# Performance work log

Measured on AMD Instinct MI355X. Metric: run time of the kernel, lower is better.

The kernel has to match this reference:

```python
import jax, jax.numpy as jnp
import numpy as np

D_K = 64
N_HEADS = 16
D_MODEL = 1024


def setup_inputs() -> dict:
    key = jax.random.key(0)
    ks = jax.random.split(key, 12)
    N, T = 2, 2048
    H = D_K * N_HEADS
    s = 1.0 / np.sqrt(D_MODEL)
    inp = {
        "q": jax.random.normal(ks[0], (N, T, D_MODEL), jnp.float32),
        "k": jax.random.normal(ks[1], (N, T, D_MODEL), jnp.float32),
        "v": jax.random.normal(ks[2], (N, T, D_MODEL), jnp.float32),
        "mask": jax.random.randint(ks[3], (N, T), 0, 2, jnp.int32),
        "Wq": jax.random.normal(ks[4], (D_MODEL, H), jnp.float32) * s,
        "bq": jax.random.normal(ks[5], (H,), jnp.float32) * 0.02,
        "Wk": jax.random.normal(ks[6], (D_MODEL, H), jnp.float32) * s,
        "bk": jax.random.normal(ks[7], (H,), jnp.float32) * 0.02,
        "Wv": jax.random.normal(ks[8], (D_MODEL, H), jnp.float32) * s,
        "bv": jax.random.normal(ks[9], (H,), jnp.float32) * 0.02,
        "Wo": jax.random.normal(ks[10], (H, D_MODEL), jnp.float32) * (1.0 / np.sqrt(H)),
        "bo": jax.random.normal(ks[11], (D_MODEL,), jnp.float32) * 0.02,
    }
    return inp


def reference(q, k, v, mask, Wq, bq, Wk, bk, Wv, bv, Wo, bo):
    N, T, _ = q.shape
    # project and split heads: [N, T, H*dk] -> [N, nH, T, dk]
    def split(x):
        return x.reshape(N, T, N_HEADS, D_K).transpose(0, 2, 1, 3)
    qh = split(q @ Wq + bq)
    kh = split(k @ Wk + bk)
    vh = split(v @ Wv + bv)
    scores = jnp.einsum("bhqd,bhkd->bhqk", qh, kh) / np.sqrt(D_K)
    # key padding mask: mask[:, None, None, :] == 0 -> -inf
    scores = jnp.where(mask[:, None, None, :] == 0, -jnp.inf, scores)
    attn = jax.nn.softmax(scores, axis=-1)
    A = jnp.einsum("bhqk,bhkd->bhqd", attn, vh)
    A = A.transpose(0, 2, 1, 3).reshape(N, T, N_HEADS * D_K)
    return A @ Wo + bo
```

## Files before the change

### kernel.cpp

```cpp
#include <hip/hip_runtime.h>

#define T_SEQ 2048
#define DM 1024
#define NH 16
#define DKH 64
#define NB 2
#define M_ROWS (NB * T_SEQ)
#define QSCALE 0.18033688011112042f

using bf16x8 = __attribute__((ext_vector_type(8))) __bf16;
using f32x4  = __attribute__((ext_vector_type(4))) float;
using halfx4 = __attribute__((ext_vector_type(4))) __fp16;
using halfx8 = __attribute__((ext_vector_type(8))) __fp16;
using halfx2 = __attribute__((ext_vector_type(2))) __fp16;
using uintx4 = __attribute__((ext_vector_type(4))) unsigned;

__device__ __forceinline__ short f2bf(float f) {
  unsigned u = __builtin_bit_cast(unsigned, f);
  u += 0x7fffu + ((u >> 16) & 1u);
  return (short)(u >> 16);
}

#if defined(__has_builtin) && __has_builtin(__builtin_amdgcn_cvt_pk_bf16_f32)
using bf16x2 = __attribute__((ext_vector_type(2))) __bf16;
__device__ __forceinline__ short2 pk2(float a, float b) {
  bf16x2 r = __builtin_amdgcn_cvt_pk_bf16_f32(a, b);
  return __builtin_bit_cast(short2, r);
}
#else
__device__ __forceinline__ short2 pk2(float a, float b) {
  short2 r; r.x = f2bf(a); r.y = f2bf(b); return r;
}
#endif

__device__ __forceinline__ short2 pkh(float a, float b) {
  halfx2 r = __builtin_amdgcn_cvt_pkrtz(a, b);
  return __builtin_bit_cast(short2, r);
}

#if defined(__has_builtin) && __has_builtin(__builtin_amdgcn_exp2f)
__device__ __forceinline__ float fexp2(float x) { return __builtin_amdgcn_exp2f(x); }
#else
__device__ __forceinline__ float fexp2(float x) { return exp2f(x); }
#endif

#if defined(__has_builtin) && __has_builtin(__builtin_amdgcn_permlane32_swap) && \
    __has_builtin(__builtin_amdgcn_permlane16_swap)
using uintx2 = __attribute__((ext_vector_type(2))) unsigned;
__device__ __forceinline__ void swap32(unsigned& a, unsigned& b) {
  uintx2 r = __builtin_amdgcn_permlane32_swap(a, b, false, false);
  a = r.x; b = r.y;
}
__device__ __forceinline__ void swap16(unsigned& a, unsigned& b) {
  uintx2 r = __builtin_amdgcn_permlane16_swap(a, b, false, false);
  a = r.x; b = r.y;
}
#else
__device__ __forceinline__ void swap32(unsigned& a, unsigned& b) {
  asm volatile("v_permlane32_swap_b32 %0, %1" : "+v"(a), "+v"(b));
}
__device__ __forceinline__ void swap16(unsigned& a, unsigned& b) {
  asm volatile("v_permlane16_swap_b32 %0, %1" : "+v"(a), "+v"(b));
}
#endif

#define GLD16(g, l)                                                            \
  __builtin_amdgcn_global_load_lds(                                            \
      (const __attribute__((address_space(1))) void*)(g),                      \
      (__attribute__((address_space(3))) void*)(l), 16, 0, 0)

__global__ __launch_bounds__(256) void prep_x(
    const float* __restrict__ q, const float* __restrict__ k,
    const float* __restrict__ v, const int* __restrict__ mask,
    short* __restrict__ dst, float* __restrict__ mf) {
  const float* s = blockIdx.z == 0 ? q : (blockIdx.z == 1 ? k : v);
  short* d = dst + (size_t)blockIdx.z * (M_ROWS * DM);
  const int n4 = M_ROWS * DM / 4;
  for (int i = blockIdx.x * 256 + threadIdx.x; i < n4; i += gridDim.x * 256) {
    float4 f = *(const float4*)(s + i * 4);
    short2 a = pk2(f.x, f.y), b = pk2(f.z, f.w);
    short4 o = {a.x, a.y, b.x, b.y};
    *(short4*)(d + i * 4) = o;
  }
  if (blockIdx.z == 0 && blockIdx.x < 4) {
    int i = (blockIdx.x * 256 + threadIdx.x) * 4;
    int4 m = *(const int4*)(mask + i);
    float4 o = {m.x ? 0.f : -1e38f, m.y ? 0.f : -1e38f,
                m.z ? 0.f : -1e38f, m.w ? 0.f : -1e38f};
    *(float4*)(mf + i) = o;
  }
}

__global__ __launch_bounds__(256) void prep_w(
    const float* __restrict__ w0, const float* __restrict__ w1,
    const float* __restrict__ w2, const float* __restrict__ w3,
    short* __restrict__ dst) {
  __shared__ short T[64][72];
  const float* W = blockIdx.z == 0 ? w0 : blockIdx.z == 1 ? w1
                   : blockIdx.z == 2 ? w2 : w3;
  short* D = dst + (size_t)blockIdx.z * (DM * DM);
  const int k0 = blockIdx.x * 64, n0 = blockIdx.y * 64;
  const int r = threadIdx.x >> 2, cs = (threadIdx.x & 3) * 16;
#pragma unroll
  for (int j = 0; j < 4; ++j) {
    float4 f = *(const float4*)(W + (size_t)(k0 + r) * DM + n0 + cs + j * 4);
    short2 a = pk2(f.x, f.y), b = pk2(f.z, f.w);
    short4 o = {a.x, a.y, b.x, b.y};
    *(short4*)&T[r][cs + j * 4] = o;
  }
  __syncthreads();
  short tmp[16];
#pragma unroll
  for (int i = 0; i < 16; ++i) tmp[i] = T[cs + i][r];
  *(int4*)(D + (size_t)(n0 + r) * DM + k0 + cs) = *(const int4*)&tmp[0];
  *(int4*)(D + (size_t)(n0 + r) * DM + k0 + cs + 8) = *(const int4*)&tmp[8];
}

__global__ __launch_bounds__(512) void gemm_qkv(
    const short* __restrict__ A_, const short* __restrict__ Bt_,
    const float* __restrict__ b0, const float* __restrict__ b1,
    const float* __restrict__ b2, short* __restrict__ Y) {
  __shared__ short As[2][4096];
  __shared__ short Bs[2][4096];
  const int z = blockIdx.z;
  const short* A = A_ + (size_t)z * (M_ROWS * DM);
  const short* Bt = Bt_ + (size_t)z * (DM * DM);
  short* Yz = Y + (size_t)z * ((size_t)M_ROWS * DM);
  const float* bias = z == 0 ? b0 : (z == 1 ? b1 : b2);
  const int m0 = blockIdx.x * 128, n0 = blockIdx.y * 128;
  const int tid = threadIdx.x, w = tid >> 6, lane = tid & 63;
  const int quad = lane >> 4, lm = lane & 15, wa = w & 1, wb = w >> 1;

  const short* Ag = A + (size_t)(m0 + w * 16 + lm) * DM + quad * 8;
  const short* Bg = Bt + (size_t)(n0 + w * 16 + lm) * DM + quad * 8;

  f32x4 acc[4][2];
#pragma unroll
  for (int i = 0; i < 4; ++i)
#pragma unroll
    for (int j = 0; j < 2; ++j) acc[i][j] = (f32x4){0.f, 0.f, 0.f, 0.f};

  GLD16(Ag, &As[0][w * 512]);
  GLD16(Bg, &Bs[0][w * 512]);

  for (int kt = 0; kt < DM / 32; ++kt) {
    const int cb = kt & 1;
    __syncthreads();
    if (kt + 1 < DM / 32) {
      GLD16(Ag + (kt + 1) * 32, &As[cb ^ 1][w * 512]);
      GLD16(Bg + (kt + 1) * 32, &Bs[cb ^ 1][w * 512]);
    }
    bf16x8 af[4], bfr[2];
#pragma unroll
    for (int i = 0; i < 4; ++i)
      af[i] = *(const bf16x8*)&As[cb][(wa * 4 + i) * 512 + quad * 128 + lm * 8];
#pragma unroll
    for (int j = 0; j < 2; ++j)
      bfr[j] = *(const bf16x8*)&Bs[cb][(wb * 2 + j) * 512 + quad * 128 + lm * 8];
#pragma unroll
    for (int mi = 0; mi < 4; ++mi)
#pragma unroll
      for (int j = 0; j < 2; ++j)
        acc[mi][j] = __builtin_amdgcn_mfma_f32_16x16x32_bf16(
            af[mi], bfr[j], acc[mi][j], 0, 0, 0);
  }

  if (z < 2) {
#pragma unroll
    for (int j = 0; j < 2; ++j) {
      const int f = n0 + (wb * 2 + j) * 16 + lm;
      const float bv = bias[f];
      const int h = f >> 6, dk = f & 63;
#pragma unroll
      for (int mi = 0; mi < 4; ++mi)
#pragma unroll
        for (int r = 0; r < 4; ++r) {
          const int m = m0 + (wa * 4 + mi) * 16 + quad * 4 + r;
          float val = acc[mi][j][r] + bv;
          if (z == 0) val *= QSCALE;
          const int b = m >> 11, tt = m & (T_SEQ - 1);
          Yz[(((size_t)(b * NH + h) << 11) + tt) * DKH + dk] = f2bf(val);
        }
    }
  } else {
#pragma unroll
    for (int j = 0; j < 2; ++j) {
      const int f = n0 + (wb * 2 + j) * 16 + lm;
      const float bv = bias[f];
      const int h = f >> 6, dk = f & 63;
#pragma unroll
      for (int mi = 0; mi < 4; ++mi) {
        const int t = m0 + (wa * 4 + mi) * 16 + quad * 4;
        const int b = t >> 11, tt = t & (T_SEQ - 1);
        short2 a = pkh(acc[mi][j][0] + bv, acc[mi][j][1] + bv);
        short2 c = pkh(acc[mi][j][2] + bv, acc[mi][j][3] + bv);
        short4 o = {a.x, a.y, c.x, c.y};
        *(short4*)(Yz + (((size_t)(b * NH + h) * DKH + dk) << 11) + tt) = o;
      }
    }
  }
}

__global__ __launch_bounds__(512) void gemm_out(
    const short* __restrict__ A, const short* __restrict__ Bt,
    const float* __restrict__ bias, float* __restrict__ Yf) {
  __shared__ short As[2][4096];
  __shared__ short Bs[2][2048];
  const int m0 = blockIdx.x * 128, n0 = blockIdx.y * 64;
  const int tid = threadIdx.x, w = tid >> 6, lane = tid & 63;
  const int quad = lane >> 4, lm = lane & 15, wa = w & 3, wb = w >> 2;

  const short* Ag = A + (size_t)(m0 + w * 16 + lm) * DM + quad * 8;
  const short* Bg = Bt + (size_t)(n0 + (w & 3) * 16 + lm) * DM + quad * 8;

  f32x4 acc[2][2];
#pragma unroll
  for (int i = 0; i < 2; ++i)
#pragma unroll
    for (int j = 0; j < 2; ++j) acc[i][j] = (f32x4){0.f, 0.f, 0.f, 0.f};

  GLD16(Ag, &As[0][w * 512]);
  if (w < 4) GLD16(Bg, &Bs[0][w * 512]);

  for (int kt = 0; kt < DM / 32; ++kt) {
    const int cb = kt & 1;
    __syncthreads();
    if (kt + 1 < DM / 32) {
      GLD16(Ag + (kt + 1) * 32, &As[cb ^ 1][w * 512]);
      if (w < 4) GLD16(Bg + (kt + 1) * 32, &Bs[cb ^ 1][w * 512]);
    }
    bf16x8 af[2], bfr[2];
#pragma unroll
    for (int i = 0; i < 2; ++i)
      af[i] = *(const bf16x8*)&As[cb][(wa * 2 + i) * 512 + quad * 128 + lm * 8];
#pragma unroll
    for (int j = 0; j < 2; ++j)
      bfr[j] = *(const bf16x8*)&Bs[cb][(wb * 2 + j) * 512 + quad * 128 + lm * 8];
#pragma unroll
    for (int mi = 0; mi < 2; ++mi)
#pragma unroll
      for (int j = 0; j < 2; ++j)
        acc[mi][j] = __builtin_amdgcn_mfma_f32_16x16x32_bf16(
            af[mi], bfr[j], acc[mi][j], 0, 0, 0);
  }

#pragma unroll
  for (int j = 0; j < 2; ++j) {
    const int n = n0 + (wb * 2 + j) * 16 + lm;
    const float bv = bias[n];
#pragma unroll
    for (int mi = 0; mi < 2; ++mi)
#pragma unroll
      for (int r = 0; r < 4; ++r) {
        const int m = m0 + (wa * 2 + mi) * 16 + quad * 4 + r;
        Yf[(size_t)m * DM + n] = acc[mi][j][r] + bv;
      }
  }
}

__global__ __launch_bounds__(512) void attn_kernel(
    const short* __restrict__ Qh, const short* __restrict__ Kh,
    const short* __restrict__ Vt, const float* __restrict__ mf,
    short* __restrict__ Ao) {
  __shared__ short Ks[2][8192];
  __shared__ short Vs[2][8192];
  const int id = blockIdx.x + gridDim.x * blockIdx.y;
  const int bh = id & 31, qt = id >> 5;
  const int b = bh >> 4, h = bh & (NH - 1);
  const int tid = threadIdx.x, w = tid >> 6, lane = tid & 63;
  const int quad = lane >> 4, lm = lane & 15;
  const size_t base = (size_t)bh * T_SEQ * DKH;
  const float* mp = mf + b * T_SEQ;
  const int q0 = qt * 128 + w * 16;

  const short* qp = Qh + base + (size_t)(q0 + lm) * DKH;
  const bf16x8 qb0 = *(const bf16x8*)(qp + quad * 8);
  const bf16x8 qb1 = *(const bf16x8*)(qp + 32 + quad * 8);

  const int sw = w & 3;
  const bool isV = w >= 4;
  const short* Kg = Kh + base + (size_t)(sw * 16 + lm) * DKH + quad * 8;
  const short* Vg = Vt + base + (size_t)(sw * 16 + lm) * T_SEQ + quad * 8;

  f32x4 ot[4];
#pragma unroll
  for (int i = 0; i < 4; ++i) ot[i] = (f32x4){0.f, 0.f, 0.f, 0.f};
  float l_part = 0.f;

  if (!isV) {
    GLD16(Kg, &Ks[0][sw * 1024]);
    GLD16(Kg + 32, &Ks[0][sw * 1024 + 512]);
    GLD16(Kg + (size_t)64 * DKH, &Ks[0][(sw + 4) * 1024]);
    GLD16(Kg + (size_t)64 * DKH + 32, &Ks[0][(sw + 4) * 1024 + 512]);
  } else {
    GLD16(Vg, &Vs[0][sw * 2048]);
    GLD16(Vg + 32, &Vs[0][sw * 2048 + 512]);
    GLD16(Vg + 64, &Vs[0][sw * 2048 + 1024]);
    GLD16(Vg + 96, &Vs[0][sw * 2048 + 1536]);
  }

  for (int kt = 0; kt < T_SEQ / 128; ++kt) {
    const int cb = kt & 1;
    const int key0 = kt * 128;
    __syncthreads();
    if (kt + 1 < T_SEQ / 128) {
      const int nk = key0 + 128;
      if (!isV) {
        GLD16(Kg + (size_t)nk * DKH, &Ks[cb ^ 1][sw * 1024]);
        GLD16(Kg + (size_t)nk * DKH + 32, &Ks[cb ^ 1][sw * 1024 + 512]);
        GLD16(Kg + (size_t)(nk + 64) * DKH, &Ks[cb ^ 1][(sw + 4) * 1024]);
        GLD16(Kg + (size_t)(nk + 64) * DKH + 32, &Ks[cb ^ 1][(sw + 4) * 1024 + 512]);
      } else {
        GLD16(Vg + nk, &Vs[cb ^ 1][sw * 2048]);
        GLD16(Vg + nk + 32, &Vs[cb ^ 1][sw * 2048 + 512]);
        GLD16(Vg + nk + 64, &Vs[cb ^ 1][sw * 2048 + 1024]);
        GLD16(Vg + nk + 96, &Vs[cb ^ 1][sw * 2048 + 1536]);
      }
    }

    halfx8 pb32[4];
#pragma unroll
    for (int kp = 0; kp < 4; ++kp) {
      unsigned pe0, pe1, po0, po1;
#pragma unroll
      for (int hf = 0; hf < 2; ++hf) {
        const int nt = kp * 2 + hf;
        bf16x8 ka0 = *(const bf16x8*)&Ks[cb][nt * 1024 + quad * 128 + lm * 8];
        bf16x8 ka1 = *(const bf16x8*)&Ks[cb][nt * 1024 + 512 + quad * 128 + lm * 8];
        f32x4 s = (f32x4){0.f, 0.f, 0.f, 0.f};
        s = __builtin_amdgcn_mfma_f32_16x16x32_bf16(ka0, qb0, s, 0, 0, 0);
        s = __builtin_amdgcn_mfma_f32_16x16x32_bf16(ka1, qb1, s, 0, 0, 0);
        const float4 m4 = *(const float4*)(mp + key0 + nt * 16 + quad * 4);
        float p0 = fexp2(s[0] + m4.x);
        float p1 = fexp2(s[1] + m4.y);
        float p2 = fexp2(s[2] + m4.z);
        float p3 = fexp2(s[3] + m4.w);
        l_part += (p0 + p1) + (p2 + p3);
        unsigned lo = __builtin_bit_cast(unsigned, pkh(p0, p1));
        unsigned hi = __builtin_bit_cast(unsigned, pkh(p2, p3));
        if (hf == 0) { pe0 = lo; pe1 = hi; } else { po0 = lo; po1 = hi; }
      }
      unsigned x0 = pe0, y0 = po0, x1 = pe1, y1 = po1;
      swap32(x0, y0); swap16(x0, y0);
      swap32(x1, y1); swap16(x1, y1);
      pb32[kp] = __builtin_bit_cast(halfx8, (uintx4){x0, x1, y0, y1});
    }

#pragma unroll
    for (int nt2 = 0; nt2 < 4; ++nt2) {
#pragma unroll
      for (int kp = 0; kp < 4; ++kp) {
        halfx8 va =
            *(const halfx8*)&Vs[cb][nt2 * 2048 + kp * 512 + quad * 128 + lm * 8];
        ot[nt2] =
            __builtin_amdgcn_mfma_f32_16x16x32_f16(va, pb32[kp], ot[nt2], 0, 0, 0);
      }
    }
  }
  l_part += __shfl_xor(l_part, 16, 64);
  l_part += __shfl_xor(l_part, 32, 64);
  const float inv = 1.f / l_part;
  const size_t row = (size_t)(b * T_SEQ + q0 + lm) * DM + h * DKH;
#pragma unroll
  for (int nt = 0; nt < 4; ++nt) {
    short2 a = pk2(ot[nt][0] * inv, ot[nt][1] * inv);
    short2 c = pk2(ot[nt][2] * inv, ot[nt][3] * inv);
    short4 o4 = {a.x, a.y, c.x, c.y};
    *(short4*)(Ao + row + nt * 16 + quad * 4) = o4;
  }
}

extern "C" void kernel_launch(void* const* d_in, const int* in_sizes, int n_in,
                              void* d_out, int out_size, void* d_ws, size_t ws_size,
                              hipStream_t stream) {
  const float* q = (const float*)d_in[0];
  const float* k = (const float*)d_in[1];
  const float* v = (const float*)d_in[2];
  const int* mk = (const int*)d_in[3];
  const float* Wq = (const float*)d_in[4];
  const float* bq = (const float*)d_in[5];
  const float* Wk = (const float*)d_in[6];
  const float* bk = (const float*)d_in[7];
  const float* Wv = (const float*)d_in[8];
  const float* bv = (const float*)d_in[9];
  const float* Wo = (const float*)d_in[10];
  const float* bo = (const float*)d_in[11];

  const size_t XE = (size_t)M_ROWS * DM;
  const size_t WE = (size_t)DM * DM;
  short* xb = (short*)d_ws;
  short* Wt = xb + 3 * XE;
  short* Qh = Wt + 4 * WE;
  float* mf = (float*)(Qh + 3 * XE);
  short* Ao = xb;

  prep_x<<<dim3(1024, 1, 3), 256, 0, stream>>>(q, k, v, mk, xb, mf);
  prep_w<<<dim3(16, 16, 4), 256, 0, stream>>>(Wq, Wk, Wv, Wo, Wt);
  gemm_qkv<<<dim3(M_ROWS / 128, DM / 128, 3), 512, 0, stream>>>(
      xb, Wt, bq, bk, bv, Qh);
  attn_kernel<<<dim3(T_SEQ / 128, NB * NH), 512, 0, stream>>>(
      Qh, Qh + XE, Qh + 2 * XE, mf, Ao);
  gemm_out<<<dim3(M_ROWS / 128, DM / 64), 512, 0, stream>>>(
      Ao, Wt + 3 * WE, bo, (float*)d_out);
}
```

Before: 256.5 us.

## Process two query tiles per wave in attention to reuse K/V tiles

Each wave now handles 32 query rows as two 16-row tiles sharing the same K and V LDS fragments, and each block covers 256 queries instead of 128. This halves K/V global loads and LDS fills per query and amortizes the LDS reads across twice the MFMA work. In exchange, accumulator and probability registers roughly double and the grid halves, which may reduce occupancy and latency hiding.

After: 254.2 us. No clear change (-0.9%).

```diff
diff --git a/kernel.cpp b/kernel.cpp
--- a/kernel.cpp
+++ b/kernel.cpp
@@ -271,21 +271,27 @@
   const int quad = lane >> 4, lm = lane & 15;
   const size_t base = (size_t)bh * T_SEQ * DKH;
   const float* mp = mf + b * T_SEQ;
-  const int q0 = qt * 128 + w * 16;
-
-  const short* qp = Qh + base + (size_t)(q0 + lm) * DKH;
-  const bf16x8 qb0 = *(const bf16x8*)(qp + quad * 8);
-  const bf16x8 qb1 = *(const bf16x8*)(qp + 32 + quad * 8);
+  const int q0 = qt * 256 + w * 32;
+
+  const short* qpA = Qh + base + (size_t)(q0 + lm) * DKH;
+  const short* qpB = qpA + (size_t)16 * DKH;
+  const bf16x8 qbA0 = *(const bf16x8*)(qpA + quad * 8);
+  const bf16x8 qbA1 = *(const bf16x8*)(qpA + 32 + quad * 8);
+  const bf16x8 qbB0 = *(const bf16x8*)(qpB + quad * 8);
+  const bf16x8 qbB1 = *(const bf16x8*)(qpB + 32 + quad * 8);
 
   const int sw = w & 3;
   const bool isV = w >= 4;
   const short* Kg = Kh + base + (size_t)(sw * 16 + lm) * DKH + quad * 8;
   const short* Vg = Vt + base + (size_t)(sw * 16 + lm) * T_SEQ + quad * 8;
 
-  f32x4 ot[4];
-#pragma unroll
-  for (int i = 0; i < 4; ++i) ot[i] = (f32x4){0.f, 0.f, 0.f, 0.f};
-  float l_part = 0.f;
+  f32x4 otA[4], otB[4];
+#pragma unroll
+  for (int i = 0; i < 4; ++i) {
+    otA[i] = (f32x4){0.f, 0.f, 0.f, 0.f};
+    otB[i] = (f32x4){0.f, 0.f, 0.f, 0.f};
+  }
+  float lA = 0.f, lB = 0.f;
 
   if (!isV) {
     GLD16(Kg, &Ks[0][sw * 1024]);
@@ -318,32 +324,55 @@
       }
     }
 
-    halfx8 pb32[4];
+    halfx8 pbA[4], pbB[4];
 #pragma unroll
     for (int kp = 0; kp < 4; ++kp) {
-      unsigned pe0, pe1, po0, po1;
+      unsigned peA0, peA1, poA0, poA1;
+      unsigned peB0, peB1, poB0, poB1;
 #pragma unroll
       for (int hf = 0; hf < 2; ++hf) {
         const int nt = kp * 2 + hf;
         bf16x8 ka0 = *(const bf16x8*)&Ks[cb][nt * 1024 + quad * 128 + lm * 8];
         bf16x8 ka1 = *(const bf16x8*)&Ks[cb][nt * 1024 + 512 + quad * 128 + lm * 8];
-        f32x4 s = (f32x4){0.f, 0.f, 0.f, 0.f};
-        s = __builtin_amdgcn_mfma_f32_16x16x32_bf16(ka0, qb0, s, 0, 0, 0);
-        s = __builtin_amdgcn_mfma_f32_16x16x32_bf16(ka1, qb1, s, 0, 0, 0);
+        f32x4 sA = (f32x4){0.f, 0.f, 0.f, 0.f};
+        sA = __builtin_amdgcn_mfma_f32_16x16x32_bf16(ka0, qbA0, sA, 0, 0, 0);
+        sA = __builtin_amdgcn_mfma_f32_16x16x32_bf16(ka1, qbA1, sA, 0, 0, 0);
+        f32x4 sB = (f32x4){0.f, 0.f, 0.f, 0.f};
+        sB = __builtin_amdgcn_mfma_f32_16x16x32_bf16(ka0, qbB0, sB, 0, 0, 0);
+        sB = __builtin_amdgcn_mfma_f32_16x16x32_bf16(ka1, qbB1, sB, 0, 0, 0);
         const float4 m4 = *(const float4*)(mp + key0 + nt * 16 + quad * 4);
-        float p0 = fexp2(s[0] + m4.x);
-        float p1 = fexp2(s[1] + m4.y);
-        float p2 = fexp2(s[2] + m4.z);
-        float p3 = fexp2(s[3] + m4.w);
-        l_part += (p0 + p1) + (p2 + p3);
-        unsigned lo = __builtin_bit_cast(unsigned, pkh(p0, p1));
-        unsigned hi = __builtin_bit_cast(unsigned, pkh(p2, p3));
-        if (hf == 0) { pe0 = lo; pe1 = hi; } else { po0 = lo; po1 = hi; }
-      }
-      unsigned x0 = pe0, y0 = po0, x1 = pe1, y1 = po1;
-      swap32(x0, y0); swap16(x0, y0);
-      swap32(x1, y1); swap16(x1, y1);
-      pb32[kp] = __builtin_bit_cast(halfx8, (uintx4){x0, x1, y0, y1});
+        float a0 = fexp2(sA[0] + m4.x);
+        float a1 = fexp2(sA[1] + m4.y);
+        float a2 = fexp2(sA[2] + m4.z);
+        float a3 = fexp2(sA[3] + m4.w);
+        lA += (a0 + a1) + (a2 + a3);
+        float b0 = fexp2(sB[0] + m4.x);
+        float b1 = fexp2(sB[1] + m4.y);
+        float b2 = fexp2(sB[2] + m4.z);
+        float b3 = fexp2(sB[3] + m4.w);
+        lB += (b0 + b1) + (b2 + b3);
+        unsigned loA = __builtin_bit_cast(unsigned, pkh(a0, a1));
+        unsigned hiA = __builtin_bit_cast(unsigned, pkh(a2, a3));
+        unsigned loB = __builtin_bit_cast(unsigned, pkh(b0, b1));
+        unsigned hiB = __builtin_bit_cast(unsigned, pkh(b2, b3));
+        if (hf == 0) {
+          peA0 = loA; peA1 = hiA; peB0 = loB; peB1 = hiB;
+        } else {
+          poA0 = loA; poA1 = hiA; poB0 = loB; poB1 = hiB;
+        }
+      }
+      {
+        unsigned x0 = peA0, y0 = poA0, x1 = peA1, y1 = poA1;
+        swap32(x0, y0); swap16(x0, y0);
+        swap32(x1, y1); swap16(x1, y1);
+        pbA[kp] = __builtin_bit_cast(halfx8, (uintx4){x0, x1, y0, y1});
+      }
+      {
+        unsigned x0 = peB0, y0 = poB0, x1 = peB1, y1 = poB1;
+        swap32(x0, y0); swap16(x0, y0);
+        swap32(x1, y1); swap16(x1, y1);
+        pbB[kp] = __builtin_bit_cast(halfx8, (uintx4){x0, x1, y0, y1});
+      }
     }
 
 #pragma unroll
@@ -352,21 +381,31 @@
       for (int kp = 0; kp < 4; ++kp) {
         halfx8 va =
             *(const halfx8*)&Vs[cb][nt2 * 2048 + kp * 512 + quad * 128 + lm * 8];
-        ot[nt2] =
-            __builtin_amdgcn_mfma_f32_16x16x32_f16(va, pb32[kp], ot[nt2], 0, 0, 0);
-      }
-    }
-  }
-  l_part += __shfl_xor(l_part, 16, 64);
-  l_part += __shfl_xor(l_part, 32, 64);
-  const float inv = 1.f / l_part;
-  const size_t row = (size_t)(b * T_SEQ + q0 + lm) * DM + h * DKH;
+        otA[nt2] =
+            __builtin_amdgcn_mfma_f32_16x16x32_f16(va, pbA[kp], otA[nt2], 0, 0, 0);
+        otB[nt2] =
+            __builtin_amdgcn_mfma_f32_16x16x32_f16(va, pbB[kp], otB[nt2], 0, 0, 0);
+      }
+    }
+  }
+  lA += __shfl_xor(lA, 16, 64);
+  lA += __shfl_xor(lA, 32, 64);
+  lB += __shfl_xor(lB, 16, 64);
+  lB += __shfl_xor(lB, 32, 64);
+  const float invA = 1.f / lA;
+  const float invB = 1.f / lB;
+  const size_t rowA = (size_t)(b * T_SEQ + q0 + lm) * DM + h * DKH;
+  const size_t rowB = rowA + (size_t)16 * DM;
 #pragma unroll
   for (int nt = 0; nt < 4; ++nt) {
-    short2 a = pk2(ot[nt][0] * inv, ot[nt][1] * inv);
-    short2 c = pk2(ot[nt][2] * inv, ot[nt][3] * inv);
+    short2 a = pk2(otA[nt][0] * invA, otA[nt][1] * invA);
+    short2 c = pk2(otA[nt][2] * invA, otA[nt][3] * invA);
     short4 o4 = {a.x, a.y, c.x, c.y};
-    *(short4*)(Ao + row + nt * 16 + quad * 4) = o4;
+    *(short4*)(Ao + rowA + nt * 16 + quad * 4) = o4;
+    short2 e = pk2(otB[nt][0] * invB, otB[nt][1] * invB);
+    short2 g = pk2(otB[nt][2] * invB, otB[nt][3] * invB);
+    short4 o5 = {e.x, e.y, g.x, g.y};
+    *(short4*)(Ao + rowB + nt * 16 + quad * 4) = o5;
   }
 }
 
@@ -398,7 +437,7 @@
   prep_w<<<dim3(16, 16, 4), 256, 0, stream>>>(Wq, Wk, Wv, Wo, Wt);
   gemm_qkv<<<dim3(M_ROWS / 128, DM / 128, 3), 512, 0, stream>>>(
       xb, Wt, bq, bk, bv, Qh);
-  attn_kernel<<<dim3(T_SEQ / 128, NB * NH), 512, 0, stream>>>(
+  attn_kernel<<<dim3(T_SEQ / 256, NB * NH), 512, 0, stream>>>(
       Qh, Qh + XE, Qh + 2 * XE, mf, Ao);
   gemm_out<<<dim3(M_ROWS / 128, DM / 64), 512, 0, stream>>>(
       Ao, Wt + 3 * WE, bo, (float*)d_out);
```
